# Optimization experiments

Hardware: AMD Instinct MI355X
Metric: run time of the kernel (lower is better)

Reference implementation:

```python
import jax, jax.numpy as jnp
import numpy as np

B, T, DNA_DIM = 8, 8192, 4
HID, C, K = 256, 5, 16
NEG = -1e30


def setup_inputs() -> dict:
    key = jax.random.key(0)
    ks = jax.random.split(key, 9)
    sequence = jax.random.normal(ks[0], (B, T, DNA_DIM), dtype=jnp.float32)
    lengths = jax.random.randint(ks[1], (B,), T // 2, T + 1).astype(jnp.int32)
    W_enc = jax.random.normal(ks[2], (DNA_DIM, HID), dtype=jnp.float32) * 0.1
    b_enc = jnp.zeros((HID,), dtype=jnp.float32)
    W_proj = jax.random.normal(ks[3], (HID, C), dtype=jnp.float32) * 0.05
    b_proj = jnp.zeros((C,), dtype=jnp.float32)
    trans = jax.random.normal(ks[4], (C, C), dtype=jnp.float32) * 0.1
    start = jax.random.normal(ks[5], (C,), dtype=jnp.float32) * 0.1
    dur = jax.random.normal(ks[6], (C, K), dtype=jnp.float32) * 0.1  # learned duration scores
    return {"sequence": sequence, "lengths": lengths, "W_enc": W_enc, "b_enc": b_enc,
            "W_proj": W_proj, "b_proj": b_proj, "trans": trans, "start": start, "dur": dur}


def reference(sequence, lengths, W_enc, b_enc, W_proj, b_proj, trans, start, dur):
    """Encoder + semi-Markov CRF head forward.

    Returns (partition, cum_scores):
      partition  : (B,) log partition function over all segmentations up to `lengths`.
      cum_scores : (B, T+1, C) cumulative per-class emission scores (segment score
                   for span (s, t] with label c is cum[t, c] - cum[s, c]).
    """
    # --- encoder: pointwise linear + GELU ---
    hidden = jax.nn.gelu(sequence @ W_enc + b_enc)          # (B, T, HID)
    emit = hidden @ W_proj + b_proj                          # (B, T, C)

    # --- cumulative segment scores ---
    cum = jnp.concatenate(
        [jnp.zeros((B, 1, C), emit.dtype), jnp.cumsum(emit, axis=1)], axis=1
    )                                                        # (B, T+1, C)

    # prevs[:, t-1, d-1, :] = cum[:, t-d, :]   (zero-padded for t-d < 0; masked by H)
    cum_pad = jnp.pad(cum, ((0, 0), (K, 0), (0, 0)))         # (B, T+1+K, C)
    prevs = jnp.stack(
        [cum_pad[:, K - d + 1: K - d + 1 + T, :] for d in range(1, K + 1)], axis=2
    )                                                        # (B, T, K, C)
    cur = cum[:, 1:, :]                                      # (B, T, C)

    dur_t = dur.T                                            # (K, C)

    # --- semi-Markov forward DP via scan; carry = last K transition-folded alphas ---
    # H[:, d-1, :] = m[t-d] where m[j, c] = logsumexp_{c'} alpha[j, c'] + trans[c', c]
    # and m[0] = start scores.
    H0 = jnp.full((B, K, C), NEG, dtype=emit.dtype).at[:, 0, :].set(start[None, :])

    def step(H, xs):
        cur_t, prev_t = xs                                   # (B, C), (B, K, C)
        seg = cur_t[:, None, :] - prev_t                     # segment emission scores
        score = H + seg + dur_t[None, :, :]                  # (B, K, C)
        alpha = jax.nn.logsumexp(score, axis=1)              # (B, C)
        m = jax.nn.logsumexp(alpha[:, :, None] + trans[None, :, :], axis=1)  # (B, C)
        Hn = jnp.concatenate([m[:, None, :], H[:, :-1, :]], axis=1)
        return Hn, alpha

    xs = (jnp.swapaxes(cur, 0, 1), jnp.swapaxes(prevs, 0, 1))
    _, alphas = jax.lax.scan(step, H0, xs)                   # (T, B, C)

    alpha_L = alphas[lengths - 1, jnp.arange(B)]             # (B, C) at each sequence end
    partition = jax.nn.logsumexp(alpha_L, axis=-1)           # (B,)
    return partition, cum
```

## Files before the change

### kernel.cpp

```cpp
#include <hip/hip_runtime.h>
#include <hip/hip_bf16.h>

#define B_ 8
#define T_ 8192
#define HID_ 256
#define C_ 5
#define K_ 16
#define NC_ 32
#define NTILE 32
#define GSPAN 272
#define NFW 15

__device__ __forceinline__ float gelu_tanh(float x) {
    float u = 0.7978845608028654f * (x + 0.044715f * x * x * x);
    float e = __expf(2.0f * u);
    float th = 1.0f - 2.0f / (e + 1.0f);
    return 0.5f * x * (1.0f + th);
}

__device__ __forceinline__ float bf16lo(unsigned int u) {
    return __uint_as_float(u << 16);
}
__device__ __forceinline__ float bf16hi(unsigned int u) {
    return __uint_as_float(u & 0xffff0000u);
}

__global__ __launch_bounds__(256) void encoder_kernel(
    const float* __restrict__ seq, const float* __restrict__ W_enc,
    const float* __restrict__ b_enc, const float* __restrict__ W_proj,
    const float* __restrict__ b_proj, float* __restrict__ emitA,
    float* __restrict__ emitB, float* __restrict__ PA)
{
    __shared__ float4 we[128];
    __shared__ float  be[128];
    __shared__ float  wp[128 * C_];
    __shared__ float  prd[4][C_];
    int tid = threadIdx.x;
    int half = blockIdx.x >> 8;
    int blk  = blockIdx.x & 255;
    int h0 = half * 128;
    if (tid < 128) {
        int h = h0 + tid;
        we[tid] = make_float4(W_enc[0*HID_+h], W_enc[1*HID_+h], W_enc[2*HID_+h], W_enc[3*HID_+h]);
        be[tid] = b_enc[h];
    }
    for (int i = tid; i < 128 * C_; i += 256) wp[i] = W_proj[h0 * C_ + i];
    __syncthreads();
    int b = blk >> 5;
    int tile = blk & 31;
    int t = tile * 256 + tid;
    float4 s = reinterpret_cast<const float4*>(seq)[(size_t)b * T_ + t];
    float a0, a1, a2, a3, a4;
    if (half == 0) { a0 = b_proj[0]; a1 = b_proj[1]; a2 = b_proj[2]; a3 = b_proj[3]; a4 = b_proj[4]; }
    else           { a0 = a1 = a2 = a3 = a4 = 0.0f; }
    #pragma unroll 8
    for (int h = 0; h < 128; ++h) {
        float4 w = we[h];
        float pre = be[h] + s.x*w.x + s.y*w.y + s.z*w.z + s.w*w.w;
        float hd = gelu_tanh(pre);
        a0 = fmaf(hd, wp[h*C_+0], a0);
        a1 = fmaf(hd, wp[h*C_+1], a1);
        a2 = fmaf(hd, wp[h*C_+2], a2);
        a3 = fmaf(hd, wp[h*C_+3], a3);
        a4 = fmaf(hd, wp[h*C_+4], a4);
    }
    float* em = half ? emitB : emitA;
    size_t base = (size_t)b * C_ * T_ + t;
    em[base + 0*T_] = a0;
    em[base + 1*T_] = a1;
    em[base + 2*T_] = a2;
    em[base + 3*T_] = a3;
    em[base + 4*T_] = a4;
    float s0 = a0, s1 = a1, s2 = a2, s3 = a3, s4 = a4;
    #pragma unroll
    for (int off = 1; off < 64; off <<= 1) {
        s0 += __shfl_xor(s0, off, 64);
        s1 += __shfl_xor(s1, off, 64);
        s2 += __shfl_xor(s2, off, 64);
        s3 += __shfl_xor(s3, off, 64);
        s4 += __shfl_xor(s4, off, 64);
    }
    int lane = tid & 63, wv = tid >> 6;
    if (lane == 0) { prd[wv][0]=s0; prd[wv][1]=s1; prd[wv][2]=s2; prd[wv][3]=s3; prd[wv][4]=s4; }
    __syncthreads();
    if (tid < C_) {
        float t4 = (prd[0][tid] + prd[1][tid]) + (prd[2][tid] + prd[3][tid]);
        PA[((half * B_ + b) * NTILE + tile) * C_ + tid] = t4;
    }
}

__global__ __launch_bounds__(64) void cumwrite_kernel(
    const float* __restrict__ emitA, const float* __restrict__ emitB,
    const float* __restrict__ PA, float* __restrict__ cum)
{
    int bx = blockIdx.x;
    int tile = bx & (NTILE - 1);
    int bc = bx >> 5;
    int b = bc / C_, c = bc - b * C_;
    int lane = threadIdx.x;
    float v = 0.0f;
    if (lane < NTILE && lane < tile)
        v = PA[((0 * B_ + b) * NTILE + lane) * C_ + c]
          + PA[((1 * B_ + b) * NTILE + lane) * C_ + c];
    #pragma unroll
    for (int o = 32; o; o >>= 1) v += __shfl_xor(v, o, 64);
    const float* eA = emitA + ((size_t)b * C_ + c) * T_;
    const float* eB = emitB + ((size_t)b * C_ + c) * T_;
    float* cb = cum + (size_t)b * (T_ + 1) * C_;
    if (tile == 0 && lane == 0) cb[c] = 0.0f;
    float carry = v;
    #pragma unroll
    for (int i = 0; i < 4; ++i) {
        int idx = tile * 256 + i * 64 + lane;
        float e = eA[idx] + eB[idx];
        float si = e;
        #pragma unroll
        for (int o = 1; o < 64; o <<= 1) {
            float n = __shfl_up(si, o, 64);
            if (lane >= o) si += n;
        }
        cb[(size_t)(idx + 1) * C_ + c] = carry + si;
        carry += __shfl(si, 63, 64);
    }
}

#define CHUNK_STEP(PP, TL)                                                    \
    {                                                                         \
        float g  = g_lds[c][16 + (TL)];                                       \
        float gi = gi_lds[c][16 + (TL)];                                      \
        P *= g; invP *= gi;                                                   \
        float d0 = 0.f, d1 = 0.f, d2 = 0.f, d3 = 0.f;                         \
        d0 = fmaf(W[0],  ed[(0  + (PP)) & 15], d0);                           \
        d1 = fmaf(W[1],  ed[(1  + (PP)) & 15], d1);                           \
        d2 = fmaf(W[2],  ed[(2  + (PP)) & 15], d2);                           \
        d3 = fmaf(W[3],  ed[(3  + (PP)) & 15], d3);                           \
        d0 = fmaf(W[4],  ed[(4  + (PP)) & 15], d0);                           \
        d1 = fmaf(W[5],  ed[(5  + (PP)) & 15], d1);                           \
        d2 = fmaf(W[6],  ed[(6  + (PP)) & 15], d2);                           \
        d3 = fmaf(W[7],  ed[(7  + (PP)) & 15], d3);                           \
        d0 = fmaf(W[8],  ed[(8  + (PP)) & 15], d0);                           \
        d1 = fmaf(W[9],  ed[(9  + (PP)) & 15], d1);                           \
        d2 = fmaf(W[10], ed[(10 + (PP)) & 15], d2);                           \
        d3 = fmaf(W[11], ed[(11 + (PP)) & 15], d3);                           \
        d0 = fmaf(W[12], ed[(12 + (PP)) & 15], d0);                           \
        d1 = fmaf(W[13], ed[(13 + (PP)) & 15], d1);                           \
        d2 = fmaf(W[14], ed[(14 + (PP)) & 15], d2);                           \
        d3 = fmaf(W[15], ed[(15 + (PP)) & 15], d3);                           \
        float dotv = (d0 + d1) + (d2 + d3);                                   \
        astep = P * dotv;                                                     \
        float A0 = __shfl(astep, base5 + 0, 64);                              \
        float A1 = __shfl(astep, base5 + 1, 64);                              \
        float A2 = __shfl(astep, base5 + 2, 64);                              \
        float A3 = __shfl(astep, base5 + 3, 64);                              \
        float A4 = __shfl(astep, base5 + 4, 64);                              \
        A0v = A0;                                                             \
        float Sn = fmaf(eT[0], A0, fmaf(eT[1], A1, fmaf(eT[2], A2,           \
                   fmaf(eT[3], A3, eT[4] * A4))));                            \
        W[15 - (PP)] = Sn * invP;                                             \
    }

#define CHUNK_RENORM()                                                        \
    {                                                                         \
        bool ok = (A0v > 1e-30f);                                             \
        float r  = ok ? __builtin_amdgcn_rcpf(A0v) : 1.0f;                    \
        float lz = ok ? __logf(A0v) : 0.0f;                                   \
        float f = P * r;                                                      \
        _Pragma("unroll") for (int q = 0; q < 16; ++q) W[q] *= f;             \
        P = 1.0f; invP = 1.0f; z += lz;                                       \
    }

#define TAIL_STEP(PP)                                                         \
    if ((PP) < rem) {                                                         \
        CHUNK_STEP(PP, tl0 + (PP));                                           \
        if ((PP) == rem - 1) Afin = astep;                                    \
        if ((((PP) & 7) == 7) && ((PP) < rem - 1)) CHUNK_RENORM();            \
    }

__global__ __launch_bounds__(448) void chunk_kernel(
    const float* __restrict__ emitA, const float* __restrict__ emitB,
    const int* __restrict__ lengths, const float* __restrict__ trans,
    const float* __restrict__ dur, __hip_bfloat16* __restrict__ Mout,
    float* __restrict__ Rout, float* __restrict__ ezOut,
    float* __restrict__ Zmx)
{
    __shared__ float g_lds[C_][GSPAN + 4];
    __shared__ float gi_lds[C_][GSPAN + 4];
    __shared__ float zsh[80];
    __shared__ float zred;
    int blk = blockIdx.x;
    int b = blk >> 5, k = blk & (NC_ - 1);
    int len = lengths[b];
    int s = (k * len) >> 5;
    int e = ((k + 1) * len) >> 5;
    int L = e - s;
    int tid = threadIdx.x;

    for (int i = tid; i < C_ * GSPAN; i += 448) {
        int cc = i / GSPAN, j = i - cc * GSPAN;
        int pos = s - 16 + j;
        float g = 1.0f, gi = 1.0f;
        if (pos >= 0 && j < 16 + L) {
            size_t gx = ((size_t)b * C_ + cc) * T_ + pos;
            float ev = emitA[gx] + emitB[gx];
            g = __expf(ev); gi = __expf(-ev);
        }
        g_lds[cc][j]  = g;
        gi_lds[cc][j] = gi;
    }
    __syncthreads();

    int lane = tid & 63, wv = tid >> 6;
    int cin = lane / 5;
    int c = lane - cin * 5;
    int col = wv * 12 + cin;
    bool active = (cin < 12) && (col < 80);
    int base5 = (cin < 12) ? (cin * 5) : 0;

    float ed[K_], eT[C_];
    #pragma unroll
    for (int j = 0; j < K_; ++j) ed[j] = __expf(dur[c * K_ + j]);
    #pragma unroll
    for (int cc = 0; cc < C_; ++cc) eT[cc] = __expf(trans[cc * C_ + c]);

    float W[K_];
    #pragma unroll
    for (int j = 0; j < K_; ++j) W[j] = 0.0f;
    if (active) {
        int j0 = col / 5;
        int c0 = col - j0 * 5;
        if (c == c0) {
            float v = 1.0f;
            for (int j = 16 - j0; j < 16; ++j) v *= g_lds[c][j];
            #pragma unroll
            for (int j = 0; j < K_; ++j) if (j == j0) W[j] = v;
        }
    }

    float P = 1.0f, invP = 1.0f, z = 0.0f, Afin = 0.0f;
    float astep = 0.0f, A0v = 0.0f;
    int nfull = (L - 1) >> 4;
    int rem = L - (nfull << 4);
    int tl0 = 0;

    for (int bi = 0; bi < nfull; ++bi) {
        CHUNK_STEP(0,  tl0 + 0);  CHUNK_STEP(1,  tl0 + 1);
        CHUNK_STEP(2,  tl0 + 2);  CHUNK_STEP(3,  tl0 + 3);
        CHUNK_STEP(4,  tl0 + 4);  CHUNK_STEP(5,  tl0 + 5);
        CHUNK_STEP(6,  tl0 + 6);  CHUNK_STEP(7,  tl0 + 7);
        CHUNK_RENORM();
        CHUNK_STEP(8,  tl0 + 8);  CHUNK_STEP(9,  tl0 + 9);
        CHUNK_STEP(10, tl0 + 10); CHUNK_STEP(11, tl0 + 11);
        CHUNK_STEP(12, tl0 + 12); CHUNK_STEP(13, tl0 + 13);
        CHUNK_STEP(14, tl0 + 14); CHUNK_STEP(15, tl0 + 15);
        CHUNK_RENORM();
        tl0 += 16;
    }
    TAIL_STEP(0);  TAIL_STEP(1);  TAIL_STEP(2);  TAIL_STEP(3);
    TAIL_STEP(4);  TAIL_STEP(5);  TAIL_STEP(6);  TAIL_STEP(7);
    TAIL_STEP(8);  TAIL_STEP(9);  TAIL_STEP(10); TAIL_STEP(11);
    TAIL_STEP(12); TAIL_STEP(13); TAIL_STEP(14); TAIL_STEP(15);

    size_t cid = (size_t)b * NC_ + k;
    if (active) {
        if (k == NC_ - 1) {
            #pragma unroll
            for (int cc2 = 0; cc2 < 1; ++cc2) { }
            Rout[(size_t)b * 400 + col * C_ + c] = Afin;
            if (c == 0) zsh[col] = z;
        } else {
            int pn = L & 15;
            float vals[K_];
            float lm = 0.0f;
            #pragma unroll
            for (int slot = 0; slot < K_; ++slot) {
                int j = (slot + pn) & 15;
                float pr = 1.0f;
                for (int i2 = 0; i2 < j; ++i2) pr *= gi_lds[c][16 + L - 1 - i2];
                float v = W[slot] * P * pr;
                vals[slot] = v;
                lm = fmaxf(lm, v);
            }
            float m0 = __shfl(lm, base5 + 0, 64);
            float m1 = __shfl(lm, base5 + 1, 64);
            float m2 = __shfl(lm, base5 + 2, 64);
            float m3 = __shfl(lm, base5 + 3, 64);
            float m4 = __shfl(lm, base5 + 4, 64);
            float cmax = fmaxf(fmaxf(fmaxf(m0, m1), fmaxf(m2, m3)), m4);
            float inv = (cmax > 0.0f) ? 1.0f / cmax : 0.0f;
            __hip_bfloat16* mb = Mout + cid * 6400 + (size_t)col * 80;
            #pragma unroll
            for (int slot = 0; slot < K_; ++slot) {
                int j = (slot + pn) & 15;
                mb[j * C_ + c] = __float2bfloat16(vals[slot] * inv);
            }
            if (c == 0) zsh[col] = (cmax > 0.0f) ? z + __logf(cmax) : -3.0e38f;
        }
    }
    __syncthreads();
    if (tid < 64) {
        float m = zsh[tid];
        if (tid < 16) m = fmaxf(m, zsh[tid + 64]);
        #pragma unroll
        for (int off = 32; off; off >>= 1) m = fmaxf(m, __shfl_xor(m, off, 64));
        if (tid == 0) zred = m;
    }
    __syncthreads();
    float zm = zred;
    if (tid == 0) Zmx[cid] = zm;
    if (active && c == 0) ezOut[cid * 80 + col] = __expf(zsh[col] - zm);
}

__global__ __launch_bounds__(320) void chain_kernel(
    const __hip_bfloat16* __restrict__ Mst, const float* __restrict__ ezZ,
    const float* __restrict__ Zmx, const float* __restrict__ Rst,
    const float* __restrict__ startv, float* __restrict__ Uvec,
    float* __restrict__ Xvec, float* __restrict__ Zu, float* __restrict__ Zx)
{
    __shared__ float Ml[2][80 * 82];
    __shared__ float vin[80], sv[80], part[4][80];
    __shared__ float red;
    int b = blockIdx.x >> 1;
    int dir = blockIdx.x & 1;
    int tid = threadIdx.x;
    float Z = 0.0f;
    int nmat = (dir == 0) ? NFW : (NC_ - 1 - NFW);

    if (dir == 0) {
        if (tid < 80) vin[tid] = (tid < C_) ? __expf(startv[tid]) : 0.0f;
        __syncthreads();
    } else {
        size_t last = (size_t)b * NC_ + NC_ - 1;
        if (tid < 80) {
            const float* R = Rst + (size_t)b * 400 + (size_t)tid * C_;
            float rs = ((R[0] + R[1]) + (R[2] + R[3])) + R[4];
            sv[tid] = rs * ezZ[last * 80 + tid];
        }
        __syncthreads();
        if (tid < 64) {
            float m = sv[tid];
            if (tid < 16) m = fmaxf(m, sv[tid + 64]);
            #pragma unroll
            for (int o = 32; o; o >>= 1) m = fmaxf(m, __shfl_xor(m, o, 64));
            if (tid == 0) red = m;
        }
        __syncthreads();
        float rm = red;
        if (tid < 80) vin[tid] = sv[tid] / rm;
        Z = Zmx[b * NC_ + NC_ - 1] + __logf(rm);
        __syncthreads();
    }

    int mk0 = (dir == 0) ? 0 : NC_ - 2;
    {
        const unsigned int* mg = (const unsigned int*)(Mst + (size_t)(b * NC_ + mk0) * 6400);
        #pragma unroll
        for (int i = 0; i < 10; ++i) {
            unsigned int u = mg[tid + 320 * i];
            int idx = (tid + 320 * i) * 2;
            int r = idx / 80, cc = idx - r * 80;
            Ml[0][r * 82 + cc]     = bf16lo(u);
            Ml[0][r * 82 + cc + 1] = bf16hi(u);
        }
    }
    __syncthreads();

    int cur = 0;
    int grp = tid / 80, r = tid - grp * 80;
    for (int it = 0; it < nmat; ++it) {
        int k  = (dir == 0) ? it : (NC_ - 2 - it);
        int kn = (dir == 0) ? k + 1 : k - 1;
        bool more = (it + 1 < nmat);
        size_t cid = (size_t)b * NC_ + k;

        unsigned int mu[10];
        if (more) {
            const unsigned int* mg = (const unsigned int*)(Mst + ((size_t)b * NC_ + kn) * 6400);
            #pragma unroll
            for (int i = 0; i < 10; ++i) mu[i] = mg[tid + 320 * i];
        }
        float ezv = 0.0f;
        if (tid < 80) {
            ezv = ezZ[cid * 80 + tid];
            sv[tid] = (dir == 0) ? vin[tid] * ezv : vin[tid];
        }
        __syncthreads();

        float p = 0.0f;
        if (dir == 0) {
            int q0 = grp * 20;
            #pragma unroll
            for (int i = 0; i < 20; ++i)
                p = fmaf(Ml[cur][(q0 + i) * 82 + r], sv[q0 + i], p);
        } else {
            int rowb = grp * 20;
            #pragma unroll
            for (int i = 0; i < 20; ++i)
                p = fmaf(Ml[cur][r * 82 + rowb + i], sv[rowb + i], p);
        }
        part[grp][r] = p;
        if (more) {
            #pragma unroll
            for (int i = 0; i < 10; ++i) {
                unsigned int u = mu[i];
                int idx = (tid + 320 * i) * 2;
                int rr = idx / 80, cc = idx - rr * 80;
                Ml[cur ^ 1][rr * 82 + cc]     = bf16lo(u);
                Ml[cur ^ 1][rr * 82 + cc + 1] = bf16hi(u);
            }
        }
        __syncthreads();

        Z += Zmx[cid];
        bool rn = ((it & 3) == 3) || (it == nmat - 1);
        if (tid < 80) {
            float nv = (part[0][tid] + part[1][tid]) + (part[2][tid] + part[3][tid]);
            if (dir == 1) nv *= ezv;
            if (rn) sv[tid] = nv; else vin[tid] = nv;
        }
        if (rn) {
            __syncthreads();
            if (tid < 64) {
                float m = sv[tid];
                if (tid < 16) m = fmaxf(m, sv[tid + 64]);
                #pragma unroll
                for (int o = 32; o; o >>= 1) m = fmaxf(m, __shfl_xor(m, o, 64));
                if (tid == 0) red = m;
            }
            __syncthreads();
            float rm = red;
            if (tid < 80) vin[tid] = sv[tid] / rm;
            Z += __logf(rm);
        }
        cur ^= 1;
    }

    if (dir == 0) {
        if (tid < 80) Xvec[b * 80 + tid] = vin[tid];
        if (tid == 0) Zx[b] = Z;
    } else {
        if (tid < 80) Uvec[b * 80 + tid] = vin[tid];
        if (tid == 0) Zu[b] = Z;
    }
}

__global__ __launch_bounds__(512) void meet_kernel(
    const float* __restrict__ Uvec, const float* __restrict__ Xvec,
    const float* __restrict__ Zu, const float* __restrict__ Zx,
    float* __restrict__ partition)
{
    int tid = threadIdx.x;
    int b = tid >> 6, lane = tid & 63;
    float v = Uvec[b * 80 + lane] * Xvec[b * 80 + lane];
    if (lane < 16) v += Uvec[b * 80 + 64 + lane] * Xvec[b * 80 + 64 + lane];
    #pragma unroll
    for (int off = 32; off; off >>= 1) v += __shfl_xor(v, off, 64);
    if (lane == 0) partition[b] = Zu[b] + Zx[b] + __logf(v);
}

extern "C" void kernel_launch(void* const* d_in, const int* in_sizes, int n_in,
                              void* d_out, int out_size, void* d_ws, size_t ws_size,
                              hipStream_t stream) {
    (void)in_sizes; (void)n_in; (void)out_size; (void)ws_size;
    const float* seq    = (const float*)d_in[0];
    const int*   lens   = (const int*)  d_in[1];
    const float* W_enc  = (const float*)d_in[2];
    const float* b_enc  = (const float*)d_in[3];
    const float* W_proj = (const float*)d_in[4];
    const float* b_proj = (const float*)d_in[5];
    const float* trans  = (const float*)d_in[6];
    const float* startv = (const float*)d_in[7];
    const float* dur    = (const float*)d_in[8];

    float* out       = (float*)d_out;
    float* partition = out;
    float* cum       = out + B_;

    float* emitA = (float*)d_ws;
    float* emitB = emitA + (size_t)B_ * C_ * T_;
    __hip_bfloat16* Mst = (__hip_bfloat16*)(emitB + (size_t)B_ * C_ * T_);
    float* Rst = (float*)(Mst + (size_t)B_ * NC_ * 6400);
    float* ezS = Rst + (size_t)B_ * 400;
    float* Zmx = ezS + (size_t)B_ * NC_ * 80;
    float* PA  = Zmx + (size_t)B_ * NC_;
    float* Uv  = PA  + 2 * B_ * NTILE * C_;
    float* Xv  = Uv  + B_ * 80;
    float* Zu  = Xv  + B_ * 80;
    float* Zx  = Zu  + B_;

    encoder_kernel<<<512, 256, 0, stream>>>(seq, W_enc, b_enc, W_proj, b_proj, emitA, emitB, PA);
    chunk_kernel<<<B_ * NC_, 448, 0, stream>>>(emitA, emitB, lens, trans, dur, Mst, Rst, ezS, Zmx);
    cumwrite_kernel<<<B_ * C_ * NTILE, 64, 0, stream>>>(emitA, emitB, PA, cum);
    chain_kernel<<<16, 320, 0, stream>>>(Mst, ezS, Zmx, Rst, startv, Uv, Xv, Zu, Zx);
    meet_kernel<<<1, 512, 0, stream>>>(Uv, Xv, Zu, Zx, partition);
}
```

Measured before the change: 91.34 us.

## Remap chunk kernel so each lane pair handles one column across five classes

The chunk kernel's thread mapping changes from one lane per (column, class), 12 columns per wave with 448 threads, to two lanes per column. Each lane carries three class states (the shared class 4 is computed redundantly by both lanes). Cross-class exchange now uses a single DPP quad-swap instead of five wave-wide shuffles per step, and the shared tables are merged into one flat buffer. The intent is to cut shuffle latency on the serial recurrence and waste fewer lanes. In exchange each thread does more FMA work and holds about three times as many registers, and the block drops to 192 threads.

```diff
diff --git a/kernel.cpp b/kernel.cpp
--- a/kernel.cpp
+++ b/kernel.cpp
@@ -9,6 +9,8 @@
 #define NC_ 32
 #define NTILE 32
 #define GSPAN 272
+#define GW 276
+#define GIOFF (5 * GW)
 #define NFW 15
 
 __device__ __forceinline__ float gelu_tanh(float x) {
@@ -23,6 +25,10 @@
 }
 __device__ __forceinline__ float bf16hi(unsigned int u) {
     return __uint_as_float(u & 0xffff0000u);
+}
+__device__ __forceinline__ float quad_swap(float x) {
+    return __uint_as_float((unsigned int)__builtin_amdgcn_mov_dpp(
+        (int)__float_as_uint(x), 0xB1, 0xF, 0xF, true));
 }
 
 __global__ __launch_bounds__(256) void encoder_kernel(
@@ -124,67 +130,83 @@
     }
 }
 
-#define CHUNK_STEP(PP, TL)                                                    \
+#define DOT16(Wr, Er, PP, OUT)                                                \
     {                                                                         \
-        float g  = g_lds[c][16 + (TL)];                                       \
-        float gi = gi_lds[c][16 + (TL)];                                      \
-        P *= g; invP *= gi;                                                   \
-        float d0 = 0.f, d1 = 0.f, d2 = 0.f, d3 = 0.f;                         \
-        d0 = fmaf(W[0],  ed[(0  + (PP)) & 15], d0);                           \
-        d1 = fmaf(W[1],  ed[(1  + (PP)) & 15], d1);                           \
-        d2 = fmaf(W[2],  ed[(2  + (PP)) & 15], d2);                           \
-        d3 = fmaf(W[3],  ed[(3  + (PP)) & 15], d3);                           \
-        d0 = fmaf(W[4],  ed[(4  + (PP)) & 15], d0);                           \
-        d1 = fmaf(W[5],  ed[(5  + (PP)) & 15], d1);                           \
-        d2 = fmaf(W[6],  ed[(6  + (PP)) & 15], d2);                           \
-        d3 = fmaf(W[7],  ed[(7  + (PP)) & 15], d3);                           \
-        d0 = fmaf(W[8],  ed[(8  + (PP)) & 15], d0);                           \
-        d1 = fmaf(W[9],  ed[(9  + (PP)) & 15], d1);                           \
-        d2 = fmaf(W[10], ed[(10 + (PP)) & 15], d2);                           \
-        d3 = fmaf(W[11], ed[(11 + (PP)) & 15], d3);                           \
-        d0 = fmaf(W[12], ed[(12 + (PP)) & 15], d0);                           \
-        d1 = fmaf(W[13], ed[(13 + (PP)) & 15], d1);                           \
-        d2 = fmaf(W[14], ed[(14 + (PP)) & 15], d2);                           \
-        d3 = fmaf(W[15], ed[(15 + (PP)) & 15], d3);                           \
-        float dotv = (d0 + d1) + (d2 + d3);                                   \
-        astep = P * dotv;                                                     \
-        float A0 = __shfl(astep, base5 + 0, 64);                              \
-        float A1 = __shfl(astep, base5 + 1, 64);                              \
-        float A2 = __shfl(astep, base5 + 2, 64);                              \
-        float A3 = __shfl(astep, base5 + 3, 64);                              \
-        float A4 = __shfl(astep, base5 + 4, 64);                              \
-        A0v = A0;                                                             \
-        float Sn = fmaf(eT[0], A0, fmaf(eT[1], A1, fmaf(eT[2], A2,           \
-                   fmaf(eT[3], A3, eT[4] * A4))));                            \
-        W[15 - (PP)] = Sn * invP;                                             \
-    }
-
-#define CHUNK_RENORM()                                                        \
+        float q0, q1, q2, q3;                                                 \
+        q0 = Wr[0] * Er[(0 + (PP)) & 15];                                     \
+        q1 = Wr[1] * Er[(1 + (PP)) & 15];                                     \
+        q2 = Wr[2] * Er[(2 + (PP)) & 15];                                     \
+        q3 = Wr[3] * Er[(3 + (PP)) & 15];                                     \
+        q0 = fmaf(Wr[4],  Er[(4  + (PP)) & 15], q0);                          \
+        q1 = fmaf(Wr[5],  Er[(5  + (PP)) & 15], q1);                          \
+        q2 = fmaf(Wr[6],  Er[(6  + (PP)) & 15], q2);                          \
+        q3 = fmaf(Wr[7],  Er[(7  + (PP)) & 15], q3);                          \
+        q0 = fmaf(Wr[8],  Er[(8  + (PP)) & 15], q0);                          \
+        q1 = fmaf(Wr[9],  Er[(9  + (PP)) & 15], q1);                          \
+        q2 = fmaf(Wr[10], Er[(10 + (PP)) & 15], q2);                          \
+        q3 = fmaf(Wr[11], Er[(11 + (PP)) & 15], q3);                          \
+        q0 = fmaf(Wr[12], Er[(12 + (PP)) & 15], q0);                          \
+        q1 = fmaf(Wr[13], Er[(13 + (PP)) & 15], q1);                          \
+        q2 = fmaf(Wr[14], Er[(14 + (PP)) & 15], q2);                          \
+        q3 = fmaf(Wr[15], Er[(15 + (PP)) & 15], q3);                          \
+        OUT = (q0 + q1) + (q2 + q3);                                          \
+    }
+
+#define CSTEP2(PP, TT)                                                        \
     {                                                                         \
-        bool ok = (A0v > 1e-30f);                                             \
-        float r  = ok ? __builtin_amdgcn_rcpf(A0v) : 1.0f;                    \
-        float lz = ok ? __logf(A0v) : 0.0f;                                   \
-        float f = P * r;                                                      \
-        _Pragma("unroll") for (int q = 0; q < 16; ++q) W[q] *= f;             \
-        P = 1.0f; invP = 1.0f; z += lz;                                       \
-    }
-
-#define TAIL_STEP(PP)                                                         \
+        float gA = gpA[(TT)], gB = gpB[(TT)], gC = gpC[(TT)];                 \
+        float hA = gpA[(TT) + GIOFF], hB = gpB[(TT) + GIOFF],                 \
+              hC = gpC[(TT) + GIOFF];                                         \
+        PA_ *= gA; PB_ *= gB; PC_ *= gC;                                      \
+        iPA *= hA; iPB *= hB; iPC *= hC;                                      \
+        float dA, dB, dC;                                                     \
+        DOT16(WA, edA, PP, dA);                                               \
+        DOT16(WB, edB, PP, dB);                                               \
+        DOT16(WC, edC, PP, dC);                                               \
+        aA = PA_ * dA; aB = PB_ * dB; aC = PC_ * dC;                          \
+        float oA = quad_swap(aA);                                             \
+        float oB = quad_swap(aB);                                             \
+        lastA0 = prodd ? oA : aA;                                             \
+        float s0 = fmaf(K0[0], aA, fmaf(K1[0], aB, fmaf(K2[0], aC,            \
+                   fmaf(K3[0], oA, K4[0] * oB))));                            \
+        float s1 = fmaf(K0[1], aA, fmaf(K1[1], aB, fmaf(K2[1], aC,            \
+                   fmaf(K3[1], oA, K4[1] * oB))));                            \
+        float s2 = fmaf(K0[2], aA, fmaf(K1[2], aB, fmaf(K2[2], aC,            \
+                   fmaf(K3[2], oA, K4[2] * oB))));                            \
+        WA[15 - (PP)] = s0 * iPA;                                             \
+        WB[15 - (PP)] = s1 * iPB;                                             \
+        WC[15 - (PP)] = s2 * iPC;                                             \
+    }
+
+#define CRENORM2()                                                            \
+    {                                                                         \
+        bool ok = (lastA0 > 1e-30f);                                          \
+        float rr = ok ? __builtin_amdgcn_rcpf(lastA0) : 1.0f;                 \
+        float lz = ok ? __logf(lastA0) : 0.0f;                                \
+        float fA = PA_ * rr, fB = PB_ * rr, fC = PC_ * rr;                    \
+        _Pragma("unroll") for (int q = 0; q < 16; ++q) {                      \
+            WA[q] *= fA; WB[q] *= fB; WC[q] *= fC;                            \
+        }                                                                     \
+        PA_ = 1.0f; PB_ = 1.0f; PC_ = 1.0f;                                   \
+        iPA = 1.0f; iPB = 1.0f; iPC = 1.0f;                                   \
+        z += lz;                                                              \
+    }
+
+#define TSTEP(PP)                                                             \
     if ((PP) < rem) {                                                         \
-        CHUNK_STEP(PP, tl0 + (PP));                                           \
-        if ((PP) == rem - 1) Afin = astep;                                    \
-        if ((((PP) & 7) == 7) && ((PP) < rem - 1)) CHUNK_RENORM();            \
-    }
-
-__global__ __launch_bounds__(448) void chunk_kernel(
+        CSTEP2(PP, tl0 + (PP));                                               \
+        if ((PP) == rem - 1) { AfA = aA; AfB = aB; AfC = aC; }                \
+        if ((((PP) & 7) == 7) && ((PP) < rem - 1)) CRENORM2();                \
+    }
+
+__global__ __launch_bounds__(192, 1) void chunk_kernel(
     const float* __restrict__ emitA, const float* __restrict__ emitB,
     const int* __restrict__ lengths, const float* __restrict__ trans,
     const float* __restrict__ dur, __hip_bfloat16* __restrict__ Mout,
     float* __restrict__ Rout, float* __restrict__ ezOut,
     float* __restrict__ Zmx)
 {
-    __shared__ float g_lds[C_][GSPAN + 4];
-    __shared__ float gi_lds[C_][GSPAN + 4];
+    __shared__ float gg[2 * 5 * GW];
     __shared__ float zsh[80];
     __shared__ float zred;
     int blk = blockIdx.x;
@@ -195,7 +217,7 @@
     int L = e - s;
     int tid = threadIdx.x;
 
-    for (int i = tid; i < C_ * GSPAN; i += 448) {
+    for (int i = tid; i < C_ * GSPAN; i += 192) {
         int cc = i / GSPAN, j = i - cc * GSPAN;
         int pos = s - 16 + j;
         float g = 1.0f, gi = 1.0f;
@@ -204,96 +226,123 @@
             float ev = emitA[gx] + emitB[gx];
             g = __expf(ev); gi = __expf(-ev);
         }
-        g_lds[cc][j]  = g;
-        gi_lds[cc][j] = gi;
+        gg[cc * GW + j] = g;
+        gg[GIOFF + cc * GW + j] = gi;
     }
     __syncthreads();
 
     int lane = tid & 63, wv = tid >> 6;
-    int cin = lane / 5;
-    int c = lane - cin * 5;
-    int col = wv * 12 + cin;
-    bool active = (cin < 12) && (col < 80);
-    int base5 = (cin < 12) ? (cin * 5) : 0;
-
-    float ed[K_], eT[C_];
+    int prodd = lane & 1;
+    int col = wv * 32 + (lane >> 1);
+    bool cstore = (col < 80);
+    int mcA = prodd ? 2 : 0;
+    int mcB = prodd ? 3 : 1;
+    int omcA = prodd ? 0 : 2;
+    int omcB = prodd ? 1 : 3;
+
+    const float* gpA = &gg[mcA * GW + 16];
+    const float* gpB = &gg[mcB * GW + 16];
+    const float* gpC = &gg[4 * GW + 16];
+
+    float edA[K_], edB[K_], edC[K_];
     #pragma unroll
-    for (int j = 0; j < K_; ++j) ed[j] = __expf(dur[c * K_ + j]);
+    for (int j = 0; j < K_; ++j) {
+        edA[j] = __expf(dur[mcA * K_ + j]);
+        edB[j] = __expf(dur[mcB * K_ + j]);
+        edC[j] = __expf(dur[4 * K_ + j]);
+    }
+    float K0[3], K1[3], K2[3], K3[3], K4[3];
+    {
+        int myc[3] = {mcA, mcB, 4};
+        #pragma unroll
+        for (int i = 0; i < 3; ++i) {
+            int c2 = myc[i];
+            K0[i] = __expf(trans[mcA  * C_ + c2]);
+            K1[i] = __expf(trans[mcB  * C_ + c2]);
+            K2[i] = __expf(trans[4    * C_ + c2]);
+            K3[i] = __expf(trans[omcA * C_ + c2]);
+            K4[i] = __expf(trans[omcB * C_ + c2]);
+        }
+    }
+
+    int j0 = col / 5, c0 = col - (col / 5) * 5;
+    float sv = 1.0f;
+    for (int j = 16 - j0; j < 16; ++j) sv *= gg[c0 * GW + j];
+    float WA[K_], WB[K_], WC[K_];
     #pragma unroll
-    for (int cc = 0; cc < C_; ++cc) eT[cc] = __expf(trans[cc * C_ + c]);
-
-    float W[K_];
-    #pragma unroll
-    for (int j = 0; j < K_; ++j) W[j] = 0.0f;
-    if (active) {
-        int j0 = col / 5;
-        int c0 = col - j0 * 5;
-        if (c == c0) {
-            float v = 1.0f;
-            for (int j = 16 - j0; j < 16; ++j) v *= g_lds[c][j];
-            #pragma unroll
-            for (int j = 0; j < K_; ++j) if (j == j0) W[j] = v;
-        }
-    }
-
-    float P = 1.0f, invP = 1.0f, z = 0.0f, Afin = 0.0f;
-    float astep = 0.0f, A0v = 0.0f;
+    for (int q = 0; q < K_; ++q) {
+        WA[q] = (c0 == mcA && q == j0) ? sv : 0.0f;
+        WB[q] = (c0 == mcB && q == j0) ? sv : 0.0f;
+        WC[q] = (c0 == 4   && q == j0) ? sv : 0.0f;
+    }
+
+    float PA_ = 1.0f, PB_ = 1.0f, PC_ = 1.0f;
+    float iPA = 1.0f, iPB = 1.0f, iPC = 1.0f;
+    float aA = 0.0f, aB = 0.0f, aC = 0.0f;
+    float AfA = 0.0f, AfB = 0.0f, AfC = 0.0f;
+    float lastA0 = 0.0f, z = 0.0f;
+
     int nfull = (L - 1) >> 4;
     int rem = L - (nfull << 4);
     int tl0 = 0;
 
     for (int bi = 0; bi < nfull; ++bi) {
-        CHUNK_STEP(0,  tl0 + 0);  CHUNK_STEP(1,  tl0 + 1);
-        CHUNK_STEP(2,  tl0 + 2);  CHUNK_STEP(3,  tl0 + 3);
-        CHUNK_STEP(4,  tl0 + 4);  CHUNK_STEP(5,  tl0 + 5);
-        CHUNK_STEP(6,  tl0 + 6);  CHUNK_STEP(7,  tl0 + 7);
-        CHUNK_RENORM();
-        CHUNK_STEP(8,  tl0 + 8);  CHUNK_STEP(9,  tl0 + 9);
-        CHUNK_STEP(10, tl0 + 10); CHUNK_STEP(11, tl0 + 11);
-        CHUNK_STEP(12, tl0 + 12); CHUNK_STEP(13, tl0 + 13);
-        CHUNK_STEP(14, tl0 + 14); CHUNK_STEP(15, tl0 + 15);
-        CHUNK_RENORM();
+        CSTEP2(0,  tl0 + 0);  CSTEP2(1,  tl0 + 1);
+        CSTEP2(2,  tl0 + 2);  CSTEP2(3,  tl0 + 3);
+        CSTEP2(4,  tl0 + 4);  CSTEP2(5,  tl0 + 5);
+        CSTEP2(6,  tl0 + 6);  CSTEP2(7,  tl0 + 7);
+        CRENORM2();
+        CSTEP2(8,  tl0 + 8);  CSTEP2(9,  tl0 + 9);
+        CSTEP2(10, tl0 + 10); CSTEP2(11, tl0 + 11);
+        CSTEP2(12, tl0 + 12); CSTEP2(13, tl0 + 13);
+        CSTEP2(14, tl0 + 14); CSTEP2(15, tl0 + 15);
+        CRENORM2();
         tl0 += 16;
     }
-    TAIL_STEP(0);  TAIL_STEP(1);  TAIL_STEP(2);  TAIL_STEP(3);
-    TAIL_STEP(4);  TAIL_STEP(5);  TAIL_STEP(6);  TAIL_STEP(7);
-    TAIL_STEP(8);  TAIL_STEP(9);  TAIL_STEP(10); TAIL_STEP(11);
-    TAIL_STEP(12); TAIL_STEP(13); TAIL_STEP(14); TAIL_STEP(15);
+    TSTEP(0);  TSTEP(1);  TSTEP(2);  TSTEP(3);
+    TSTEP(4);  TSTEP(5);  TSTEP(6);  TSTEP(7);
+    TSTEP(8);  TSTEP(9);  TSTEP(10); TSTEP(11);
+    TSTEP(12); TSTEP(13); TSTEP(14); TSTEP(15);
 
     size_t cid = (size_t)b * NC_ + k;
-    if (active) {
-        if (k == NC_ - 1) {
-            #pragma unroll
-            for (int cc2 = 0; cc2 < 1; ++cc2) { }
-            Rout[(size_t)b * 400 + col * C_ + c] = Afin;
-            if (c == 0) zsh[col] = z;
-        } else {
-            int pn = L & 15;
-            float vals[K_];
-            float lm = 0.0f;
-            #pragma unroll
-            for (int slot = 0; slot < K_; ++slot) {
-                int j = (slot + pn) & 15;
-                float pr = 1.0f;
-                for (int i2 = 0; i2 < j; ++i2) pr *= gi_lds[c][16 + L - 1 - i2];
-                float v = W[slot] * P * pr;
-                vals[slot] = v;
-                lm = fmaxf(lm, v);
+    int pn = L & 15;
+    if (k == NC_ - 1) {
+        if (cstore) {
+            float* rb = Rout + (size_t)b * 400 + (size_t)col * C_;
+            rb[mcA] = AfA;
+            rb[mcB] = AfB;
+            if (prodd) rb[4] = AfC;
+            if (!prodd) zsh[col] = z;
+        }
+    } else {
+        float lm = 0.0f;
+        #pragma unroll
+        for (int slot = 0; slot < K_; ++slot) {
+            int j = (slot + pn) & 15;
+            float p1 = 1.0f, p2 = 1.0f, p3 = 1.0f;
+            for (int i2 = 0; i2 < j; ++i2) {
+                p1 *= gg[GIOFF + mcA * GW + 16 + L - 1 - i2];
+                p2 *= gg[GIOFF + mcB * GW + 16 + L - 1 - i2];
+                p3 *= gg[GIOFF + 4   * GW + 16 + L - 1 - i2];
             }
-            float m0 = __shfl(lm, base5 + 0, 64);
-            float m1 = __shfl(lm, base5 + 1, 64);
-            float m2 = __shfl(lm, base5 + 2, 64);
-            float m3 = __shfl(lm, base5 + 3, 64);
-            float m4 = __shfl(lm, base5 + 4, 64);
-            float cmax = fmaxf(fmaxf(fmaxf(m0, m1), fmaxf(m2, m3)), m4);
-            float inv = (cmax > 0.0f) ? 1.0f / cmax : 0.0f;
+            float vA = WA[slot] * PA_ * p1;
+            float vB = WB[slot] * PB_ * p2;
+            float vC = WC[slot] * PC_ * p3;
+            WA[slot] = vA; WB[slot] = vB; WC[slot] = vC;
+            lm = fmaxf(lm, fmaxf(fmaxf(vA, vB), vC));
+        }
+        float cmax = fmaxf(lm, quad_swap(lm));
+        float inv = (cmax > 0.0f) ? 1.0f / cmax : 0.0f;
+        if (cstore) {
             __hip_bfloat16* mb = Mout + cid * 6400 + (size_t)col * 80;
             #pragma unroll
             for (int slot = 0; slot < K_; ++slot) {
                 int j = (slot + pn) & 15;
-                mb[j * C_ + c] = __float2bfloat16(vals[slot] * inv);
+                mb[j * C_ + mcA] = __float2bfloat16(WA[slot] * inv);
+                mb[j * C_ + mcB] = __float2bfloat16(WB[slot] * inv);
+                if (prodd) mb[j * C_ + 4] = __float2bfloat16(WC[slot] * inv);
             }
-            if (c == 0) zsh[col] = (cmax > 0.0f) ? z + __logf(cmax) : -3.0e38f;
+            if (!prodd) zsh[col] = (cmax > 0.0f) ? z + __logf(cmax) : -3.0e38f;
         }
     }
     __syncthreads();
@@ -307,7 +356,7 @@
     __syncthreads();
     float zm = zred;
     if (tid == 0) Zmx[cid] = zm;
-    if (active && c == 0) ezOut[cid * 80 + col] = __expf(zsh[col] - zm);
+    if (cstore && !prodd) ezOut[cid * 80 + col] = __expf(zsh[col] - zm);
 }
 
 __global__ __launch_bounds__(320) void chain_kernel(
@@ -488,7 +537,7 @@
     float* Zx  = Zu  + B_;
 
     encoder_kernel<<<512, 256, 0, stream>>>(seq, W_enc, b_enc, W_proj, b_proj, emitA, emitB, PA);
-    chunk_kernel<<<B_ * NC_, 448, 0, stream>>>(emitA, emitB, lens, trans, dur, Mst, Rst, ezS, Zmx);
+    chunk_kernel<<<B_ * NC_, 192, 0, stream>>>(emitA, emitB, lens, trans, dur, Mst, Rst, ezS, Zmx);
     cumwrite_kernel<<<B_ * C_ * NTILE, 64, 0, stream>>>(emitA, emitB, PA, cum);
     chain_kernel<<<16, 320, 0, stream>>>(Mst, ezS, Zmx, Rst, startv, Uv, Xv, Zu, Zx);
     meet_kernel<<<1, 512, 0, stream>>>(Uv, Xv, Zu, Zx, partition);
```

Result: slower. 233.6 us (+155.7%).

## Remap chunk lanes to 8-wide groups and use DPP instead of shuffles

Applied to the files above, without the earlier changes.

The chunk kernel's thread mapping changes from groups of 5 lanes per column (12 per wave, 448 threads) to aligned groups of 8 lanes per column (8 per wave, 640 threads). This lets the per-step cross-class exchange use DPP quad and row moves instead of five ds_bpermute shuffles, with lanes 4-7 cooperatively computing class 4's transition sum. The g and gi LDS reads become float4 vector loads every four steps, and no lanes are left idle for inactive columns. The cost is more threads per block, redundant work in lanes 5-7, and a more intricate cross-lane reduction.

```diff
diff --git a/kernel.cpp b/kernel.cpp
--- a/kernel.cpp
+++ b/kernel.cpp
@@ -9,6 +9,8 @@
 #define NC_ 32
 #define NTILE 32
 #define GSPAN 272
+#define GW 276
+#define GIOFF (5 * GW)
 #define NFW 15
 
 __device__ __forceinline__ float gelu_tanh(float x) {
@@ -23,6 +25,11 @@
 }
 __device__ __forceinline__ float bf16hi(unsigned int u) {
     return __uint_as_float(u & 0xffff0000u);
+}
+template <int CTRL>
+__device__ __forceinline__ float dppf(float x) {
+    return __uint_as_float((unsigned int)__builtin_amdgcn_mov_dpp(
+        (int)__float_as_uint(x), CTRL, 0xF, 0xF, true));
 }
 
 __global__ __launch_bounds__(256) void encoder_kernel(
@@ -124,67 +131,89 @@
     }
 }
 
-#define CHUNK_STEP(PP, TL)                                                    \
+#define DOT16(PP, OUT)                                                        \
     {                                                                         \
-        float g  = g_lds[c][16 + (TL)];                                       \
-        float gi = gi_lds[c][16 + (TL)];                                      \
-        P *= g; invP *= gi;                                                   \
-        float d0 = 0.f, d1 = 0.f, d2 = 0.f, d3 = 0.f;                         \
-        d0 = fmaf(W[0],  ed[(0  + (PP)) & 15], d0);                           \
-        d1 = fmaf(W[1],  ed[(1  + (PP)) & 15], d1);                           \
-        d2 = fmaf(W[2],  ed[(2  + (PP)) & 15], d2);                           \
-        d3 = fmaf(W[3],  ed[(3  + (PP)) & 15], d3);                           \
-        d0 = fmaf(W[4],  ed[(4  + (PP)) & 15], d0);                           \
-        d1 = fmaf(W[5],  ed[(5  + (PP)) & 15], d1);                           \
-        d2 = fmaf(W[6],  ed[(6  + (PP)) & 15], d2);                           \
-        d3 = fmaf(W[7],  ed[(7  + (PP)) & 15], d3);                           \
-        d0 = fmaf(W[8],  ed[(8  + (PP)) & 15], d0);                           \
-        d1 = fmaf(W[9],  ed[(9  + (PP)) & 15], d1);                           \
-        d2 = fmaf(W[10], ed[(10 + (PP)) & 15], d2);                           \
-        d3 = fmaf(W[11], ed[(11 + (PP)) & 15], d3);                           \
-        d0 = fmaf(W[12], ed[(12 + (PP)) & 15], d0);                           \
-        d1 = fmaf(W[13], ed[(13 + (PP)) & 15], d1);                           \
-        d2 = fmaf(W[14], ed[(14 + (PP)) & 15], d2);                           \
-        d3 = fmaf(W[15], ed[(15 + (PP)) & 15], d3);                           \
-        float dotv = (d0 + d1) + (d2 + d3);                                   \
-        astep = P * dotv;                                                     \
-        float A0 = __shfl(astep, base5 + 0, 64);                              \
-        float A1 = __shfl(astep, base5 + 1, 64);                              \
-        float A2 = __shfl(astep, base5 + 2, 64);                              \
-        float A3 = __shfl(astep, base5 + 3, 64);                              \
-        float A4 = __shfl(astep, base5 + 4, 64);                              \
-        A0v = A0;                                                             \
-        float Sn = fmaf(eT[0], A0, fmaf(eT[1], A1, fmaf(eT[2], A2,           \
-                   fmaf(eT[3], A3, eT[4] * A4))));                            \
-        W[15 - (PP)] = Sn * invP;                                             \
-    }
-
-#define CHUNK_RENORM()                                                        \
+        float q0, q1, q2, q3;                                                 \
+        q0 = W[0] * ed[(0 + (PP)) & 15];                                      \
+        q1 = W[1] * ed[(1 + (PP)) & 15];                                      \
+        q2 = W[2] * ed[(2 + (PP)) & 15];                                      \
+        q3 = W[3] * ed[(3 + (PP)) & 15];                                      \
+        q0 = fmaf(W[4],  ed[(4  + (PP)) & 15], q0);                           \
+        q1 = fmaf(W[5],  ed[(5  + (PP)) & 15], q1);                           \
+        q2 = fmaf(W[6],  ed[(6  + (PP)) & 15], q2);                           \
+        q3 = fmaf(W[7],  ed[(7  + (PP)) & 15], q3);                           \
+        q0 = fmaf(W[8],  ed[(8  + (PP)) & 15], q0);                           \
+        q1 = fmaf(W[9],  ed[(9  + (PP)) & 15], q1);                           \
+        q2 = fmaf(W[10], ed[(10 + (PP)) & 15], q2);                           \
+        q3 = fmaf(W[11], ed[(11 + (PP)) & 15], q3);                           \
+        q0 = fmaf(W[12], ed[(12 + (PP)) & 15], q0);                           \
+        q1 = fmaf(W[13], ed[(13 + (PP)) & 15], q1);                           \
+        q2 = fmaf(W[14], ed[(14 + (PP)) & 15], q2);                           \
+        q3 = fmaf(W[15], ed[(15 + (PP)) & 15], q3);                           \
+        OUT = (q0 + q1) + (q2 + q3);                                          \
+    }
+
+#define CSTEP(PP, GV, GIV)                                                    \
     {                                                                         \
-        bool ok = (A0v > 1e-30f);                                             \
-        float r  = ok ? __builtin_amdgcn_rcpf(A0v) : 1.0f;                    \
-        float lz = ok ? __logf(A0v) : 0.0f;                                   \
-        float f = P * r;                                                      \
+        P *= (GV); iP *= (GIV);                                               \
+        float dtv;                                                            \
+        DOT16(PP, dtv);                                                       \
+        acur = P * dtv;                                                       \
+        float t1 = dppf<0xB1>(acur);                                          \
+        float t2 = dppf<0x4E>(acur);                                          \
+        float t3 = dppf<0x1B>(acur);                                          \
+        float t4 = dppf<0x141>(acur);                                         \
+        lastA4 = isq1 ? acur : t4;                                            \
+        float sn0 = fmaf(w0, acur, w1 * t1) + fmaf(w2, t2, w3 * t3)           \
+                  + w4 * t4;                                                  \
+        float pq = fmaf(wself, acur, wtm * t4);                               \
+        pq += dppf<0xB1>(pq);                                                 \
+        pq += dppf<0x4E>(pq);                                                 \
+        float Sn = isq1 ? pq : sn0;                                           \
+        W[15 - (PP)] = Sn * iP;                                               \
+    }
+
+#define CRENORM()                                                             \
+    {                                                                         \
+        bool ok = (lastA4 > 1e-30f);                                          \
+        float rr = ok ? __builtin_amdgcn_rcpf(lastA4) : 1.0f;                 \
+        float lz = ok ? __logf(lastA4) : 0.0f;                                \
+        float f = P * rr;                                                     \
         _Pragma("unroll") for (int q = 0; q < 16; ++q) W[q] *= f;             \
-        P = 1.0f; invP = 1.0f; z += lz;                                       \
-    }
-
-#define TAIL_STEP(PP)                                                         \
+        P = 1.0f; iP = 1.0f; z += lz;                                         \
+    }
+
+#define QBLK(Q)                                                               \
+    {                                                                         \
+        float4 vg  = *reinterpret_cast<const float4*>(gpg + tl0 + (Q));       \
+        float4 vgi = *reinterpret_cast<const float4*>(gpi + tl0 + (Q));       \
+        CSTEP((Q)+0, vg.x, vgi.x); CSTEP((Q)+1, vg.y, vgi.y);                 \
+        CSTEP((Q)+2, vg.z, vgi.z); CSTEP((Q)+3, vg.w, vgi.w);                 \
+    }
+
+#define TS(PP, GV, GIV)                                                       \
     if ((PP) < rem) {                                                         \
-        CHUNK_STEP(PP, tl0 + (PP));                                           \
-        if ((PP) == rem - 1) Afin = astep;                                    \
-        if ((((PP) & 7) == 7) && ((PP) < rem - 1)) CHUNK_RENORM();            \
-    }
-
-__global__ __launch_bounds__(448) void chunk_kernel(
+        CSTEP(PP, GV, GIV);                                                   \
+        if ((PP) == rem - 1) Af = acur;                                       \
+        if ((((PP) & 7) == 7) && ((PP) < rem - 1)) CRENORM();                 \
+    }
+
+#define TQ(Q)                                                                 \
+    if ((Q) < rem) {                                                          \
+        float4 vg  = *reinterpret_cast<const float4*>(gpg + tl0 + (Q));       \
+        float4 vgi = *reinterpret_cast<const float4*>(gpi + tl0 + (Q));       \
+        TS((Q)+0, vg.x, vgi.x); TS((Q)+1, vg.y, vgi.y);                       \
+        TS((Q)+2, vg.z, vgi.z); TS((Q)+3, vg.w, vgi.w);                       \
+    }
+
+__global__ __launch_bounds__(640) void chunk_kernel(
     const float* __restrict__ emitA, const float* __restrict__ emitB,
     const int* __restrict__ lengths, const float* __restrict__ trans,
     const float* __restrict__ dur, __hip_bfloat16* __restrict__ Mout,
     float* __restrict__ Rout, float* __restrict__ ezOut,
     float* __restrict__ Zmx)
 {
-    __shared__ float g_lds[C_][GSPAN + 4];
-    __shared__ float gi_lds[C_][GSPAN + 4];
+    __shared__ float gg[2 * 5 * GW];
     __shared__ float zsh[80];
     __shared__ float zred;
     int blk = blockIdx.x;
@@ -195,7 +224,7 @@
     int L = e - s;
     int tid = threadIdx.x;
 
-    for (int i = tid; i < C_ * GSPAN; i += 448) {
+    for (int i = tid; i < C_ * GSPAN; i += 640) {
         int cc = i / GSPAN, j = i - cc * GSPAN;
         int pos = s - 16 + j;
         float g = 1.0f, gi = 1.0f;
@@ -204,97 +233,91 @@
             float ev = emitA[gx] + emitB[gx];
             g = __expf(ev); gi = __expf(-ev);
         }
-        g_lds[cc][j]  = g;
-        gi_lds[cc][j] = gi;
+        gg[cc * GW + j] = g;
+        gg[GIOFF + cc * GW + j] = gi;
     }
     __syncthreads();
 
     int lane = tid & 63, wv = tid >> 6;
-    int cin = lane / 5;
-    int c = lane - cin * 5;
-    int col = wv * 12 + cin;
-    bool active = (cin < 12) && (col < 80);
-    int base5 = (cin < 12) ? (cin * 5) : 0;
-
-    float ed[K_], eT[C_];
+    int grp = lane >> 3;
+    int sub = lane & 7;
+    int col = wv * 8 + grp;
+    bool isq1 = (sub >= 4);
+    int c = isq1 ? 4 : sub;
+
+    const float* gpg = &gg[c * GW + 16];
+    const float* gpi = &gg[GIOFF + c * GW + 16];
+
+    float ed[K_];
     #pragma unroll
     for (int j = 0; j < K_; ++j) ed[j] = __expf(dur[c * K_ + j]);
-    #pragma unroll
-    for (int cc = 0; cc < C_; ++cc) eT[cc] = __expf(trans[cc * C_ + c]);
-
+
+    float w0 = 0.f, w1 = 0.f, w2 = 0.f, w3 = 0.f, w4 = 0.f;
+    float wtm = 0.f, wself = 0.f;
+    if (!isq1) {
+        w0 = __expf(trans[c * C_ + c]);
+        w1 = __expf(trans[(c ^ 1) * C_ + c]);
+        w2 = __expf(trans[(c ^ 2) * C_ + c]);
+        w3 = __expf(trans[(c ^ 3) * C_ + c]);
+        w4 = __expf(trans[4 * C_ + c]);
+    } else {
+        wtm = __expf(trans[(sub ^ 7) * C_ + 4]);
+        wself = (sub == 4) ? __expf(trans[4 * C_ + 4]) : 0.0f;
+    }
+
+    int j0 = col / 5, c0 = col - j0 * 5;
+    float sv = 1.0f;
+    for (int j = 16 - j0; j < 16; ++j) sv *= gg[c0 * GW + j];
     float W[K_];
     #pragma unroll
-    for (int j = 0; j < K_; ++j) W[j] = 0.0f;
-    if (active) {
-        int j0 = col / 5;
-        int c0 = col - j0 * 5;
-        if (c == c0) {
-            float v = 1.0f;
-            for (int j = 16 - j0; j < 16; ++j) v *= g_lds[c][j];
-            #pragma unroll
-            for (int j = 0; j < K_; ++j) if (j == j0) W[j] = v;
-        }
-    }
-
-    float P = 1.0f, invP = 1.0f, z = 0.0f, Afin = 0.0f;
-    float astep = 0.0f, A0v = 0.0f;
+    for (int q = 0; q < K_; ++q) W[q] = (c == c0 && q == j0) ? sv : 0.0f;
+
+    float P = 1.0f, iP = 1.0f, z = 0.0f;
+    float acur = 0.0f, Af = 0.0f, lastA4 = 0.0f;
+
     int nfull = (L - 1) >> 4;
     int rem = L - (nfull << 4);
     int tl0 = 0;
 
     for (int bi = 0; bi < nfull; ++bi) {
-        CHUNK_STEP(0,  tl0 + 0);  CHUNK_STEP(1,  tl0 + 1);
-        CHUNK_STEP(2,  tl0 + 2);  CHUNK_STEP(3,  tl0 + 3);
-        CHUNK_STEP(4,  tl0 + 4);  CHUNK_STEP(5,  tl0 + 5);
-        CHUNK_STEP(6,  tl0 + 6);  CHUNK_STEP(7,  tl0 + 7);
-        CHUNK_RENORM();
-        CHUNK_STEP(8,  tl0 + 8);  CHUNK_STEP(9,  tl0 + 9);
-        CHUNK_STEP(10, tl0 + 10); CHUNK_STEP(11, tl0 + 11);
-        CHUNK_STEP(12, tl0 + 12); CHUNK_STEP(13, tl0 + 13);
-        CHUNK_STEP(14, tl0 + 14); CHUNK_STEP(15, tl0 + 15);
-        CHUNK_RENORM();
+        QBLK(0); QBLK(4);
+        CRENORM();
+        QBLK(8); QBLK(12);
+        CRENORM();
         tl0 += 16;
     }
-    TAIL_STEP(0);  TAIL_STEP(1);  TAIL_STEP(2);  TAIL_STEP(3);
-    TAIL_STEP(4);  TAIL_STEP(5);  TAIL_STEP(6);  TAIL_STEP(7);
-    TAIL_STEP(8);  TAIL_STEP(9);  TAIL_STEP(10); TAIL_STEP(11);
-    TAIL_STEP(12); TAIL_STEP(13); TAIL_STEP(14); TAIL_STEP(15);
+    TQ(0); TQ(4); TQ(8); TQ(12);
 
     size_t cid = (size_t)b * NC_ + k;
-    if (active) {
-        if (k == NC_ - 1) {
-            #pragma unroll
-            for (int cc2 = 0; cc2 < 1; ++cc2) { }
-            Rout[(size_t)b * 400 + col * C_ + c] = Afin;
-            if (c == 0) zsh[col] = z;
-        } else {
-            int pn = L & 15;
-            float vals[K_];
-            float lm = 0.0f;
-            #pragma unroll
-            for (int slot = 0; slot < K_; ++slot) {
-                int j = (slot + pn) & 15;
-                float pr = 1.0f;
-                for (int i2 = 0; i2 < j; ++i2) pr *= gi_lds[c][16 + L - 1 - i2];
-                float v = W[slot] * P * pr;
-                vals[slot] = v;
-                lm = fmaxf(lm, v);
-            }
-            float m0 = __shfl(lm, base5 + 0, 64);
-            float m1 = __shfl(lm, base5 + 1, 64);
-            float m2 = __shfl(lm, base5 + 2, 64);
-            float m3 = __shfl(lm, base5 + 3, 64);
-            float m4 = __shfl(lm, base5 + 4, 64);
-            float cmax = fmaxf(fmaxf(fmaxf(m0, m1), fmaxf(m2, m3)), m4);
-            float inv = (cmax > 0.0f) ? 1.0f / cmax : 0.0f;
+    int pn = L & 15;
+    if (k == NC_ - 1) {
+        if (sub < C_) Rout[(size_t)b * 400 + (size_t)col * C_ + c] = Af;
+        if (sub == 0) zsh[col] = z;
+    } else {
+        float lm = 0.0f;
+        #pragma unroll
+        for (int slot = 0; slot < K_; ++slot) {
+            int j = (slot + pn) & 15;
+            float pr = 1.0f;
+            for (int i2 = 0; i2 < j; ++i2)
+                pr *= gg[GIOFF + c * GW + 16 + L - 1 - i2];
+            float vv = W[slot] * P * pr;
+            W[slot] = vv;
+            lm = fmaxf(lm, vv);
+        }
+        float m1 = fmaxf(lm, dppf<0xB1>(lm));
+        float m2 = fmaxf(m1, dppf<0x4E>(m1));
+        float cmax = fmaxf(m2, dppf<0x141>(m2));
+        float inv = (cmax > 0.0f) ? 1.0f / cmax : 0.0f;
+        if (sub < C_) {
             __hip_bfloat16* mb = Mout + cid * 6400 + (size_t)col * 80;
             #pragma unroll
             for (int slot = 0; slot < K_; ++slot) {
                 int j = (slot + pn) & 15;
-                mb[j * C_ + c] = __float2bfloat16(vals[slot] * inv);
+                mb[j * C_ + c] = __float2bfloat16(W[slot] * inv);
             }
-            if (c == 0) zsh[col] = (cmax > 0.0f) ? z + __logf(cmax) : -3.0e38f;
-        }
+        }
+        if (sub == 0) zsh[col] = (cmax > 0.0f) ? z + __logf(cmax) : -3.0e38f;
     }
     __syncthreads();
     if (tid < 64) {
@@ -307,7 +330,7 @@
     __syncthreads();
     float zm = zred;
     if (tid == 0) Zmx[cid] = zm;
-    if (active && c == 0) ezOut[cid * 80 + col] = __expf(zsh[col] - zm);
+    if (sub == 0) ezOut[cid * 80 + col] = __expf(zsh[col] - zm);
 }
 
 __global__ __launch_bounds__(320) void chain_kernel(
@@ -488,7 +511,7 @@
     float* Zx  = Zu  + B_;
 
     encoder_kernel<<<512, 256, 0, stream>>>(seq, W_enc, b_enc, W_proj, b_proj, emitA, emitB, PA);
-    chunk_kernel<<<B_ * NC_, 448, 0, stream>>>(emitA, emitB, lens, trans, dur, Mst, Rst, ezS, Zmx);
+    chunk_kernel<<<B_ * NC_, 640, 0, stream>>>(emitA, emitB, lens, trans, dur, Mst, Rst, ezS, Zmx);
     cumwrite_kernel<<<B_ * C_ * NTILE, 64, 0, stream>>>(emitA, emitB, PA, cum);
     chain_kernel<<<16, 320, 0, stream>>>(Mst, ezS, Zmx, Rst, startv, Uv, Xv, Zu, Zx);
     meet_kernel<<<1, 512, 0, stream>>>(Uv, Xv, Zu, Zx, partition);
```

After: 125.1 us. +37.0%, slower.
